# Performance work log

Hardware: AMD Instinct MI355X
Metric: run time of the kernel (lower is better)

Reference implementation:

```python
import jax, jax.numpy as jnp
import numpy as np

N = 50000      # nodes
E = 800000     # directed edges (before self loops)
IN = 128       # in_channels
H = 4          # heads
C = 64         # hidden_channels per head
G = 64         # graphs in batch
SLOPE = 0.2    # PyG GATConv default negative_slope


def setup_inputs() -> dict:
    key = jax.random.key(0)
    ks = jax.random.split(key, 16)
    x = jax.random.normal(ks[0], (N, IN), jnp.float32)
    edge_index = jax.random.randint(ks[1], (2, E), 0, N, dtype=jnp.int32)
    batch = jnp.sort(jax.random.randint(ks[2], (N,), 0, G, dtype=jnp.int32))
    s_in = 1.0 / np.sqrt(IN)
    s_hid = 1.0 / np.sqrt(H * C)
    return {
        "x": x,
        "edge_index": edge_index,
        "batch": batch,
        # layer 1: GATConv(IN -> C, heads=H, concat)
        "W1": jax.random.normal(ks[3], (IN, H * C), jnp.float32) * s_in,
        "a_src1": jax.random.normal(ks[4], (H, C), jnp.float32) * s_hid,
        "a_dst1": jax.random.normal(ks[5], (H, C), jnp.float32) * s_hid,
        "b1": jnp.zeros((H * C,), jnp.float32),
        # layer 2: GATConv(H*C -> C, heads=H, concat)
        "W2": jax.random.normal(ks[6], (H * C, H * C), jnp.float32) * s_hid,
        "a_src2": jax.random.normal(ks[7], (H, C), jnp.float32) * s_hid,
        "a_dst2": jax.random.normal(ks[8], (H, C), jnp.float32) * s_hid,
        "b2": jnp.zeros((H * C,), jnp.float32),
        # classifier head
        "W_lin": jax.random.normal(ks[9], (H * C, 2), jnp.float32) * s_hid,
        "b_lin": jnp.zeros((2,), jnp.float32),
    }


def _gat_conv(x, src, dst, W, a_src, a_dst, b):
    """PyG-style GATConv (concat heads, self-loops already in src/dst)."""
    n = x.shape[0]
    h = (x @ W).reshape(n, H, C)                       # [n, H, C]
    alpha_s = jnp.einsum('nhc,hc->nh', h, a_src)       # [n, H]
    alpha_d = jnp.einsum('nhc,hc->nh', h, a_dst)
    e = alpha_s[src] + alpha_d[dst]                    # [Etot, H]
    e = jnp.where(e > 0, e, SLOPE * e)                 # LeakyReLU
    # segment softmax over edges incoming to each destination node
    e_max = jax.lax.stop_gradient(jax.ops.segment_max(e, dst, num_segments=n))
    ex = jnp.exp(e - e_max[dst])
    denom = jax.ops.segment_sum(ex, dst, num_segments=n)
    alpha = ex / denom[dst]                            # [Etot, H]
    msg = alpha[:, :, None] * h[src]                   # [Etot, H, C]
    out = jax.ops.segment_sum(msg, dst, num_segments=n)
    return out.reshape(n, H * C) + b


def reference(x, edge_index, batch, W1, a_src1, a_dst1, b1,
              W2, a_src2, a_dst2, b2, W_lin, b_lin):
    n = x.shape[0]
    # add self loops (PyG GATConv default add_self_loops=True)
    loop = jnp.arange(n, dtype=edge_index.dtype)
    src = jnp.concatenate([edge_index[0], loop])
    dst = jnp.concatenate([edge_index[1], loop])

    h = _gat_conv(x, src, dst, W1, a_src1, a_dst1, b1)
    h = jax.nn.elu(h)                                  # dropout inactive (eval)
    h = _gat_conv(h, src, dst, W2, a_src2, a_dst2, b2)
    h = jax.nn.elu(h)

    # global mean pool over node-to-graph assignment
    sums = jax.ops.segment_sum(h, batch, num_segments=G)
    cnt = jax.ops.segment_sum(jnp.ones((n,), h.dtype), batch, num_segments=G)
    pooled = sums / jnp.maximum(cnt, 1.0)[:, None]     # [G, H*C]

    return pooled @ W_lin + b_lin                      # [G, 2] logits
```

## Files before the change

kernel.cpp:

```cpp
#include <hip/hip_runtime.h>
#include <hip/hip_bf16.h>
#include <math.h>

#define NN 50000
#define EE 800000
#define IN_CH 128
#define HH 4
#define CC 64
#define GG 64
#define HC 256
#define SLOPE 0.2f

#define NBUK 98
#define BDST 512
#define CAPB 10240
#define CAPD 64

typedef short bf16x8 __attribute__((ext_vector_type(8)));
typedef float f32x4  __attribute__((ext_vector_type(4)));
typedef float f32x2  __attribute__((ext_vector_type(2)));

__device__ inline ushort f2bf(float f) {
    union { __hip_bfloat16 h; ushort u; } c;
    c.h = __float2bfloat16(f);
    return c.u;
}
__device__ inline float bfu(ushort u) {
    union { uint u; float f; } c; c.u = ((uint)u) << 16; return c.f;
}
__device__ inline uchar f2e4m3(float v) {
    return (uchar)(__builtin_amdgcn_cvt_pk_fp8_f32(v, v, 0, false) & 0xff);
}
__device__ inline void pkfma(f32x2& a, f32x2 b, f32x2 c) {
    asm("v_pk_fma_f32 %0, %1, %2, %0" : "+v"(a) : "v"(b), "v"(c));
}


__global__ void init_kernel(int* __restrict__ bcnt,
                            float* __restrict__ pool, float* __restrict__ pcnt) {
    int i = blockIdx.x * blockDim.x + threadIdx.x;
    if (i < NBUK) bcnt[i] = 0;
    if (i < GG * HC) pool[i] = 0.f;
    if (i < GG) pcnt[i] = 0.f;
}


__global__ __launch_bounds__(256) void partition_kernel(const int* __restrict__ ei,
                                                        int* __restrict__ bcnt,
                                                        int2* __restrict__ part,
                                                        int total) {
    __shared__ int hist[NBUK];
    __shared__ int base[NBUK];
    int t = threadIdx.x;
    int c0 = blockIdx.x * 2048;
    for (int b = t; b < NBUK; b += 256) hist[b] = 0;
    __syncthreads();
    int s[8], d[8], rk[8], bk[8];
    #pragma unroll
    for (int k = 0; k < 8; ++k) {
        int i = c0 + k * 256 + t;
        rk[k] = -1;
        if (i < total) {
            if (i < EE) { s[k] = ei[i]; d[k] = ei[EE + i]; }
            else        { s[k] = d[k] = i - EE; }
            bk[k] = d[k] >> 9;
            rk[k] = atomicAdd(&hist[bk[k]], 1);
        }
    }
    __syncthreads();
    for (int b = t; b < NBUK; b += 256) {
        int h = hist[b];
        base[b] = h ? atomicAdd(&bcnt[b], h) : 0;
    }
    __syncthreads();
    #pragma unroll
    for (int k = 0; k < 8; ++k) {
        if (rk[k] >= 0) {
            int pos = base[bk[k]] + rk[k];
            if (pos < CAPB)
                part[(size_t)bk[k] * CAPB + pos] = make_int2(s[k], d[k]);
        }
    }
}


__global__ __launch_bounds__(1024) void bucket_csr_kernel(const int* __restrict__ bcnt,
                                                          const int2* __restrict__ part,
                                                          ushort* __restrict__ csrb,
                                                          int* __restrict__ cnt_out, int n) {
    __shared__ int cnt[BDST];
    int b = blockIdx.x, t = threadIdx.x;
    int d0 = b << 9;
    for (int i = t; i < BDST; i += 1024) cnt[i] = 0;
    __syncthreads();
    int m = min(bcnt[b], CAPB);
    const int2* pp = part + (size_t)b * CAPB;
    for (int i = t; i < m; i += 1024) {
        int2 e = pp[i];
        int ld = e.y - d0;
        int r = atomicAdd(&cnt[ld], 1);
        if (r < CAPD)
            csrb[((size_t)(d0 + ld) << 6) + r] = (ushort)e.x;
    }
    __syncthreads();
    for (int i = t; i < BDST; i += 1024) {
        int dd = d0 + i;
        if (dd < n) cnt_out[dd] = min(cnt[i], CAPD);
    }
}


__global__ __launch_bounds__(256) void convert_w_kernel(const float* __restrict__ B,
                                                        ushort* __restrict__ Bt, int K) {
    __shared__ float tile[32][33];
    int kt = blockIdx.x;
    int n0 = blockIdx.y * 32;
    int tx = threadIdx.x & 31, ty = threadIdx.x >> 5;
    #pragma unroll
    for (int r = ty; r < 32; r += 8)
        tile[r][tx] = B[(size_t)(kt * 32 + r) * 256 + n0 + tx];
    __syncthreads();
    #pragma unroll
    for (int r = ty; r < 32; r += 8)
        Bt[((size_t)kt * 256 + n0 + r) * 32 + tx] = f2bf(tile[tx][r]);
}


template <int K, bool A_BF16>
__global__ __launch_bounds__(256) void mfma_gemm_fused(const void* __restrict__ Ap,
                                                       const ushort* __restrict__ Bt,
                                                       uchar* __restrict__ H8,
                                                       float* __restrict__ as_,
                                                       float* __restrict__ ad_,
                                                       const float* __restrict__ a_src,
                                                       const float* __restrict__ a_dst,
                                                       int M) {
    __shared__ __align__(16) ushort As[64 * 32];
    __shared__ __align__(16) ushort Bs[256 * 32];
    int tid = threadIdx.x;
    int wave = tid >> 6, lane = tid & 63;
    int bm = blockIdx.x * 64;

    f32x4 acc[4][4] = {{}};

    for (int k0 = 0; k0 < K; k0 += 32) {
        {
            int row = tid >> 2, sl = tid & 3;
            int gr = bm + row;
            uint4 q = {0u, 0u, 0u, 0u};
            if (gr < M) {
                if constexpr (A_BF16) {
                    q = *reinterpret_cast<const uint4*>((const ushort*)Ap + (size_t)gr * K + k0 + sl * 8);
                } else {
                    const float* ap = (const float*)Ap + (size_t)gr * K + k0 + sl * 8;
                    float4 f0 = *reinterpret_cast<const float4*>(ap);
                    float4 f1 = *reinterpret_cast<const float4*>(ap + 4);
                    q.x = (uint)f2bf(f0.x) | ((uint)f2bf(f0.y) << 16);
                    q.y = (uint)f2bf(f0.z) | ((uint)f2bf(f0.w) << 16);
                    q.z = (uint)f2bf(f1.x) | ((uint)f2bf(f1.y) << 16);
                    q.w = (uint)f2bf(f1.z) | ((uint)f2bf(f1.w) << 16);
                }
            }
            int ssl = sl ^ ((row >> 1) & 3);
            *reinterpret_cast<uint4*>(&As[row * 32 + ssl * 8]) = q;
        }
        {
            const ushort* bt = Bt + (size_t)(k0 >> 5) * (256 * 32);
            #pragma unroll
            for (int cI = 0; cI < 4; ++cI) {
                int idx = cI * 256 + tid;
                uint4 v = *reinterpret_cast<const uint4*>(bt + idx * 8);
                int n = idx >> 2, sl = idx & 3;
                int ssl = sl ^ ((n >> 1) & 3);
                *reinterpret_cast<uint4*>(&Bs[n * 32 + ssl * 8]) = v;
            }
        }
        __syncthreads();

        int r16 = lane & 15, kg = lane >> 4;
        bf16x8 af[4], bfr[4];
        #pragma unroll
        for (int mi = 0; mi < 4; ++mi) {
            int row = mi * 16 + r16;
            int ssl = kg ^ ((row >> 1) & 3);
            af[mi] = *reinterpret_cast<const bf16x8*>(&As[row * 32 + ssl * 8]);
        }
        #pragma unroll
        for (int ni = 0; ni < 4; ++ni) {
            int n = wave * 64 + ni * 16 + r16;
            int ssl = kg ^ ((n >> 1) & 3);
            bfr[ni] = *reinterpret_cast<const bf16x8*>(&Bs[n * 32 + ssl * 8]);
        }
        #pragma unroll
        for (int mi = 0; mi < 4; ++mi)
            #pragma unroll
            for (int ni = 0; ni < 4; ++ni)
                acc[mi][ni] = __builtin_amdgcn_mfma_f32_16x16x32_bf16(af[mi], bfr[ni], acc[mi][ni], 0, 0, 0);
        __syncthreads();
    }

    int r16 = lane & 15, rg = lane >> 4;
    float asv[4], adv[4];
    #pragma unroll
    for (int ni = 0; ni < 4; ++ni) {
        asv[ni] = a_src[wave * 64 + ni * 16 + r16];
        adv[ni] = a_dst[wave * 64 + ni * 16 + r16];
    }
    #pragma unroll
    for (int mi = 0; mi < 4; ++mi) {
        #pragma unroll
        for (int r = 0; r < 4; ++r) {
            int row = bm + mi * 16 + rg * 4 + r;
            float ps = 0.f, pd = 0.f;
            if (row < M) {
                #pragma unroll
                for (int ni = 0; ni < 4; ++ni) {
                    float v = acc[mi][ni][r];
                    H8[(size_t)row * HC + wave * 64 + ni * 16 + r16] = f2e4m3(v);
                    ps += v * asv[ni];
                    pd += v * adv[ni];
                }
            }
            #pragma unroll
            for (int o = 1; o < 16; o <<= 1) {
                ps += __shfl_xor(ps, o, 64);
                pd += __shfl_xor(pd, o, 64);
            }
            if (row < M && r16 == 0) {
                as_[row * HH + wave] = ps;
                ad_[row * HH + wave] = pd;
            }
        }
    }
}


template <bool OUT_BF16>
__global__ __launch_bounds__(256) void aggregate14_kernel(const uchar* __restrict__ h8,
                                                          const float* __restrict__ as_,
                                                          const float* __restrict__ ad_,
                                                          const int* __restrict__ cnt,
                                                          const ushort* __restrict__ csrb,
                                                          const float* __restrict__ bias,
                                                          void* __restrict__ outp, int n) {
    int w = threadIdx.x >> 6, lane = threadIdx.x & 63;
    int dst = blockIdx.x * 4 + w;
    if (dst >= n) return;
    int es = lane >> 2, hh = lane & 3;
    int ep = lane >> 5, cl = lane & 31;
    int hsel = cl >> 3;

    __shared__ int2 s_pk[4][64][4];

    int deg = cnt[dst];
    int degp = (deg + 7) & ~7;
    const ushort* srcs = csrb + ((size_t)dst << 6);
    float ad = ad_[dst * HH + hh];

    f32x2 accp[4] = {};
    const char* hb = (const char*)h8 + cl * 8;

    int ntile = (degp + 15) >> 4;

    {
        float ew[4]; int sw[4];
        float lm = -INFINITY;
        #pragma unroll
        for (int t = 0; t < 4; ++t) {
            int j = t * 16 + es;
            float e = -INFINITY; int s = 0;
            if (t < ntile && j < deg) {
                s = (int)srcs[j];
                float tv = as_[s * HH + hh] + ad;
                e = fmaxf(tv, tv * SLOPE);
            }
            ew[t] = e; sw[t] = s;
            lm = fmaxf(lm, e);
        }
        #pragma unroll
        for (int o = 4; o < 64; o <<= 1) lm = fmaxf(lm, __shfl_xor(lm, o, 64));
        float den = 0.f;
        #pragma unroll
        for (int t = 0; t < 4; ++t) {
            float wgt = __expf(ew[t] - lm);
            ew[t] = wgt; den += wgt;
        }
        #pragma unroll
        for (int o = 4; o < 64; o <<= 1) den += __shfl_xor(den, o, 64);
        float invden = 1.f / den;
        #pragma unroll
        for (int t = 0; t < 4; ++t) {
            int j = t * 16 + es;
            if (t < ntile && j < degp) {
                s_pk[w][j][hh] = make_int2(__float_as_int(ew[t] * invden), sw[t] << 8);
            }
        }
    }

#define LOADPK(off_, vv, al)                                             \
    {                                                                    \
        int2 pk_ = s_pk[w][jj + (off_) + ep][hsel];                      \
        al = __int_as_float(pk_.x);                                      \
        vv = *reinterpret_cast<const uint2*>(hb + pk_.y);                \
    }

#define DECODE_PK(vv, al)                                                \
    {                                                                    \
        f32x2 ap_; ap_[0] = al; ap_[1] = al;                             \
        f32x2 f_;                                                        \
        f_ = __builtin_amdgcn_cvt_pk_f32_fp8((int)(vv).x, false);        \
        pkfma(accp[0], f_, ap_);                                         \
        f_ = __builtin_amdgcn_cvt_pk_f32_fp8((int)(vv).x, true);         \
        pkfma(accp[1], f_, ap_);                                         \
        f_ = __builtin_amdgcn_cvt_pk_f32_fp8((int)(vv).y, false);        \
        pkfma(accp[2], f_, ap_);                                         \
        f_ = __builtin_amdgcn_cvt_pk_f32_fp8((int)(vv).y, true);         \
        pkfma(accp[3], f_, ap_);                                         \
    }

    for (int jj = 0; jj < degp; jj += 8) {
        uint2 v0, v1, v2, v3;
        float a0, a1, a2, a3;
        LOADPK(0, v0, a0)
        LOADPK(2, v1, a1)
        LOADPK(4, v2, a2)
        LOADPK(6, v3, a3)
        DECODE_PK(v0, a0)
        DECODE_PK(v1, a1)
        DECODE_PK(v2, a2)
        DECODE_PK(v3, a3)
    }
#undef LOADPK
#undef DECODE_PK

    float lo[4] = {accp[0][0], accp[0][1], accp[1][0], accp[1][1]};
    float hi[4] = {accp[2][0], accp[2][1], accp[3][0], accp[3][1]};
    float fin[4];
    #pragma unroll
    for (int k = 0; k < 4; ++k) {
        float send = ep ? lo[k] : hi[k];
        float recv = __shfl_xor(send, 32, 64);
        fin[k] = (ep ? hi[k] : lo[k]) + recv;
    }

    int ch = cl * 8 + ep * 4;
    const float4 b4 = *reinterpret_cast<const float4*>(bias + ch);
    float r0 = fin[0] + b4.x, r1 = fin[1] + b4.y, r2 = fin[2] + b4.z, r3 = fin[3] + b4.w;
    r0 = r0 > 0.f ? r0 : __expf(r0) - 1.f;
    r1 = r1 > 0.f ? r1 : __expf(r1) - 1.f;
    r2 = r2 > 0.f ? r2 : __expf(r2) - 1.f;
    r3 = r3 > 0.f ? r3 : __expf(r3) - 1.f;
    if constexpr (OUT_BF16) {
        uint2 q;
        q.x = (uint)f2bf(r0) | ((uint)f2bf(r1) << 16);
        q.y = (uint)f2bf(r2) | ((uint)f2bf(r3) << 16);
        *reinterpret_cast<uint2*>((ushort*)outp + (size_t)dst * HC + ch) = q;
    } else {
        *reinterpret_cast<float4*>((float*)outp + (size_t)dst * HC + ch) =
            make_float4(r0, r1, r2, r3);
    }
}


__global__ __launch_bounds__(256) void pool_kernel(const ushort* __restrict__ o,
                                                   const int* __restrict__ batch,
                                                   float* __restrict__ pool,
                                                   float* __restrict__ pcnt, int n) {
    int t = threadIdx.x;
    int start = blockIdx.x * 64;
    if (start >= n) return;
    int endn = min(start + 64, n);
    int g = batch[start];
    float acc = 0.f;
    int cnt = 0;
    for (int node = start; node < endn; ++node) {
        int gb = batch[node];
        if (gb != g) {
            atomicAdd(&pool[g * HC + t], acc);
            if (t == 0) atomicAdd(&pcnt[g], (float)cnt);
            acc = 0.f; cnt = 0; g = gb;
        }
        acc += bfu(o[(size_t)node * HC + t]);
        cnt++;
    }
    atomicAdd(&pool[g * HC + t], acc);
    if (t == 0) atomicAdd(&pcnt[g], (float)cnt);
}

__global__ __launch_bounds__(256) void head_kernel(const float* __restrict__ pool,
                                                   const float* __restrict__ pcnt,
                                                   const float* __restrict__ Wl,
                                                   const float* __restrict__ bl,
                                                   float* __restrict__ out) {
    int g = blockIdx.x;
    int t = threadIdx.x;
    float inv = 1.f / fmaxf(pcnt[g], 1.f);
    float p = pool[g * HC + t] * inv;
    float v0 = p * Wl[t * 2 + 0];
    float v1 = p * Wl[t * 2 + 1];
    #pragma unroll
    for (int o = 32; o > 0; o >>= 1) {
        v0 += __shfl_down(v0, o, 64);
        v1 += __shfl_down(v1, o, 64);
    }
    __shared__ float s0[4], s1[4];
    int wid = t >> 6, lane = t & 63;
    if (lane == 0) { s0[wid] = v0; s1[wid] = v1; }
    __syncthreads();
    if (t == 0) {
        out[g * 2 + 0] = s0[0] + s0[1] + s0[2] + s0[3] + bl[0];
        out[g * 2 + 1] = s1[0] + s1[1] + s1[2] + s1[3] + bl[1];
    }
}


extern "C" void kernel_launch(void* const* d_in, const int* in_sizes, int n_in,
                              void* d_out, int out_size, void* d_ws, size_t ws_size,
                              hipStream_t stream) {
    const float* x    = (const float*)d_in[0];
    const int*   ei   = (const int*)d_in[1];
    const int*   batch= (const int*)d_in[2];
    const float* W1   = (const float*)d_in[3];
    const float* as1  = (const float*)d_in[4];
    const float* ad1  = (const float*)d_in[5];
    const float* b1   = (const float*)d_in[6];
    const float* W2   = (const float*)d_in[7];
    const float* as2  = (const float*)d_in[8];
    const float* ad2  = (const float*)d_in[9];
    const float* b2   = (const float*)d_in[10];
    const float* Wl   = (const float*)d_in[11];
    const float* bl   = (const float*)d_in[12];
    float* out = (float*)d_out;

    char* ws = (char*)d_ws;
    size_t off_b = 0;
    auto alloc = [&](size_t bytes) -> void* {
        void* p = ws + off_b;
        off_b = (off_b + bytes + 255) & ~(size_t)255;
        return p;
    };
    uchar*  h8   = (uchar*)alloc((size_t)NN * HC);
    ushort* o1   = (ushort*)alloc((size_t)NN * HC * 2);
    ushort* o2   = (ushort*)alloc((size_t)NN * HC * 2);
    float*  as_  = (float*)alloc((size_t)NN * HH * 4);
    float*  ad_  = (float*)alloc((size_t)NN * HH * 4);
    int*    bcnt = (int*)alloc((size_t)NBUK * 4);
    int2*   part = (int2*)alloc((size_t)NBUK * CAPB * 8);
    ushort* csrb = (ushort*)alloc((size_t)NN * CAPD * 2);
    int*    cnt  = (int*)alloc((size_t)NN * 4);
    float*  pool = (float*)alloc((size_t)GG * HC * 4);
    float*  pcnt = (float*)alloc((size_t)GG * 4);
    ushort* Bt1  = (ushort*)alloc((size_t)HC * IN_CH * 2);
    ushort* Bt2  = (ushort*)alloc((size_t)HC * HC * 2);
    if (off_b > ws_size) return;

    const int TOTAL = EE + NN;

    init_kernel<<<(GG * HC + 255) / 256, 256, 0, stream>>>(bcnt, pool, pcnt);
    partition_kernel<<<(TOTAL + 2047) / 2048, 256, 0, stream>>>(ei, bcnt, part, TOTAL);
    bucket_csr_kernel<<<NBUK, 1024, 0, stream>>>(bcnt, part, csrb, cnt, NN);

    convert_w_kernel<<<dim3(IN_CH / 32, 8), 256, 0, stream>>>(W1, Bt1, IN_CH);
    convert_w_kernel<<<dim3(HC / 32, 8), 256, 0, stream>>>(W2, Bt2, HC);

    int gblocks = (NN + 63) / 64;
    int ablocks = (NN + 3) / 4;
    mfma_gemm_fused<IN_CH, false><<<gblocks, 256, 0, stream>>>(x, Bt1, h8, as_, ad_, as1, ad1, NN);
    aggregate14_kernel<true><<<ablocks, 256, 0, stream>>>(h8, as_, ad_, cnt, csrb, b1, o1, NN);
    mfma_gemm_fused<HC, true><<<gblocks, 256, 0, stream>>>(o1, Bt2, h8, as_, ad_, as2, ad2, NN);
    aggregate14_kernel<true><<<ablocks, 256, 0, stream>>>(h8, as_, ad_, cnt, csrb, b2, o2, NN);
    pool_kernel<<<(NN + 63) / 64, 256, 0, stream>>>(o2, batch, pool, pcnt, NN);
    head_kernel<<<GG, 256, 0, stream>>>(pool, pcnt, Wl, bl, out);
}
```

Measured before the change: 192.4 us.

## Merge prep kernels, stage CSR rows in LDS, fuse pooling with head

Combines bucket-counter init and both weight transposes into one prep kernel. Builds per-bucket CSR rows in shared memory and writes them out with coalesced 16-byte stores. Replaces the atomic pool kernel and the head kernel with a single per-graph kernel that binary-searches the sorted batch array and sums its node range. This reduces launches and scattered writes, but pooling now runs on only 64 blocks with a serial loop per graph, and bucket_csr uses 64KB of LDS.

```diff
diff --git a/kernel.cpp b/kernel.cpp
--- a/kernel.cpp
+++ b/kernel.cpp
@@ -36,12 +36,34 @@
 }
 
 
-__global__ void init_kernel(int* __restrict__ bcnt,
-                            float* __restrict__ pool, float* __restrict__ pcnt) {
-    int i = blockIdx.x * blockDim.x + threadIdx.x;
-    if (i < NBUK) bcnt[i] = 0;
-    if (i < GG * HC) pool[i] = 0.f;
-    if (i < GG) pcnt[i] = 0.f;
+__device__ void conv_body(const float* __restrict__ B, ushort* __restrict__ Bt,
+                          int kt, int n0, float (*tile)[33]) {
+    int tx = threadIdx.x & 31, ty = threadIdx.x >> 5;
+    #pragma unroll
+    for (int r = ty; r < 32; r += 8)
+        tile[r][tx] = B[(size_t)(kt * 32 + r) * 256 + n0 + tx];
+    __syncthreads();
+    #pragma unroll
+    for (int r = ty; r < 32; r += 8)
+        Bt[((size_t)kt * 256 + n0 + r) * 32 + tx] = f2bf(tile[tx][r]);
+}
+
+__global__ __launch_bounds__(256) void prep_kernel(const float* __restrict__ W1,
+                                                   ushort* __restrict__ Bt1,
+                                                   const float* __restrict__ W2,
+                                                   ushort* __restrict__ Bt2,
+                                                   int* __restrict__ bcnt) {
+    __shared__ float tile[32][33];
+    int b = blockIdx.x;
+    if (b < 32) {
+        conv_body(W1, Bt1, b >> 3, (b & 7) * 32, tile);
+    } else if (b < 96) {
+        int bb = b - 32;
+        conv_body(W2, Bt2, bb >> 3, (bb & 7) * 32, tile);
+    } else {
+        int i = threadIdx.x;
+        if (i < NBUK) bcnt[i] = 0;
+    }
 }
 
 
@@ -89,6 +111,7 @@
                                                           ushort* __restrict__ csrb,
                                                           int* __restrict__ cnt_out, int n) {
     __shared__ int cnt[BDST];
+    __shared__ ushort rows[BDST * CAPD];
     int b = blockIdx.x, t = threadIdx.x;
     int d0 = b << 9;
     for (int i = t; i < BDST; i += 1024) cnt[i] = 0;
@@ -99,30 +122,17 @@
         int2 e = pp[i];
         int ld = e.y - d0;
         int r = atomicAdd(&cnt[ld], 1);
-        if (r < CAPD)
-            csrb[((size_t)(d0 + ld) << 6) + r] = (ushort)e.x;
-    }
-    __syncthreads();
+        if (r < CAPD) rows[(ld << 6) + r] = (ushort)e.x;
+    }
+    __syncthreads();
+    const uint4* src4 = reinterpret_cast<const uint4*>(rows);
+    uint4* dst4 = reinterpret_cast<uint4*>(csrb + ((size_t)d0 << 6));
+    #pragma unroll
+    for (int i = 0; i < 4; ++i) dst4[i * 1024 + t] = src4[i * 1024 + t];
     for (int i = t; i < BDST; i += 1024) {
         int dd = d0 + i;
         if (dd < n) cnt_out[dd] = min(cnt[i], CAPD);
     }
-}
-
-
-__global__ __launch_bounds__(256) void convert_w_kernel(const float* __restrict__ B,
-                                                        ushort* __restrict__ Bt, int K) {
-    __shared__ float tile[32][33];
-    int kt = blockIdx.x;
-    int n0 = blockIdx.y * 32;
-    int tx = threadIdx.x & 31, ty = threadIdx.x >> 5;
-    #pragma unroll
-    for (int r = ty; r < 32; r += 8)
-        tile[r][tx] = B[(size_t)(kt * 32 + r) * 256 + n0 + tx];
-    __syncthreads();
-    #pragma unroll
-    for (int r = ty; r < 32; r += 8)
-        Bt[((size_t)kt * 256 + n0 + r) * 32 + tx] = f2bf(tile[tx][r]);
 }
 
 
@@ -362,46 +372,32 @@
 }
 
 
-__global__ __launch_bounds__(256) void pool_kernel(const ushort* __restrict__ o,
-                                                   const int* __restrict__ batch,
-                                                   float* __restrict__ pool,
-                                                   float* __restrict__ pcnt, int n) {
-    int t = threadIdx.x;
-    int start = blockIdx.x * 64;
-    if (start >= n) return;
-    int endn = min(start + 64, n);
-    int g = batch[start];
-    float acc = 0.f;
-    int cnt = 0;
-    for (int node = start; node < endn; ++node) {
-        int gb = batch[node];
-        if (gb != g) {
-            atomicAdd(&pool[g * HC + t], acc);
-            if (t == 0) atomicAdd(&pcnt[g], (float)cnt);
-            acc = 0.f; cnt = 0; g = gb;
-        }
-        acc += bfu(o[(size_t)node * HC + t]);
-        cnt++;
-    }
-    atomicAdd(&pool[g * HC + t], acc);
-    if (t == 0) atomicAdd(&pcnt[g], (float)cnt);
-}
-
-__global__ __launch_bounds__(256) void head_kernel(const float* __restrict__ pool,
-                                                   const float* __restrict__ pcnt,
-                                                   const float* __restrict__ Wl,
-                                                   const float* __restrict__ bl,
-                                                   float* __restrict__ out) {
+__global__ __launch_bounds__(256) void pool_head_kernel(const ushort* __restrict__ o,
+                                                        const int* __restrict__ batch,
+                                                        const float* __restrict__ Wl,
+                                                        const float* __restrict__ bl,
+                                                        float* __restrict__ out, int n) {
     int g = blockIdx.x;
     int t = threadIdx.x;
-    float inv = 1.f / fmaxf(pcnt[g], 1.f);
-    float p = pool[g * HC + t] * inv;
+    int lo = 0, hi = n;
+    while (lo < hi) { int mid = (lo + hi) >> 1; if (batch[mid] < g) lo = mid + 1; else hi = mid; }
+    int start = lo;
+    hi = n;
+    while (lo < hi) { int mid = (lo + hi) >> 1; if (batch[mid] < g + 1) lo = mid + 1; else hi = mid; }
+    int end = lo;
+
+    float acc = 0.f;
+    #pragma unroll 4
+    for (int node = start; node < end; ++node)
+        acc += bfu(o[(size_t)node * HC + t]);
+    float inv = 1.f / fmaxf((float)(end - start), 1.f);
+    float p = acc * inv;
     float v0 = p * Wl[t * 2 + 0];
     float v1 = p * Wl[t * 2 + 1];
     #pragma unroll
-    for (int o = 32; o > 0; o >>= 1) {
-        v0 += __shfl_down(v0, o, 64);
-        v1 += __shfl_down(v1, o, 64);
+    for (int off = 32; off > 0; off >>= 1) {
+        v0 += __shfl_down(v0, off, 64);
+        v1 += __shfl_down(v1, off, 64);
     }
     __shared__ float s0[4], s1[4];
     int wid = t >> 6, lane = t & 63;
@@ -446,22 +442,17 @@
     float*  ad_  = (float*)alloc((size_t)NN * HH * 4);
     int*    bcnt = (int*)alloc((size_t)NBUK * 4);
     int2*   part = (int2*)alloc((size_t)NBUK * CAPB * 8);
-    ushort* csrb = (ushort*)alloc((size_t)NN * CAPD * 2);
+    ushort* csrb = (ushort*)alloc((size_t)NBUK * BDST * CAPD * 2);
     int*    cnt  = (int*)alloc((size_t)NN * 4);
-    float*  pool = (float*)alloc((size_t)GG * HC * 4);
-    float*  pcnt = (float*)alloc((size_t)GG * 4);
     ushort* Bt1  = (ushort*)alloc((size_t)HC * IN_CH * 2);
     ushort* Bt2  = (ushort*)alloc((size_t)HC * HC * 2);
     if (off_b > ws_size) return;
 
     const int TOTAL = EE + NN;
 
-    init_kernel<<<(GG * HC + 255) / 256, 256, 0, stream>>>(bcnt, pool, pcnt);
+    prep_kernel<<<97, 256, 0, stream>>>(W1, Bt1, W2, Bt2, bcnt);
     partition_kernel<<<(TOTAL + 2047) / 2048, 256, 0, stream>>>(ei, bcnt, part, TOTAL);
     bucket_csr_kernel<<<NBUK, 1024, 0, stream>>>(bcnt, part, csrb, cnt, NN);
-
-    convert_w_kernel<<<dim3(IN_CH / 32, 8), 256, 0, stream>>>(W1, Bt1, IN_CH);
-    convert_w_kernel<<<dim3(HC / 32, 8), 256, 0, stream>>>(W2, Bt2, HC);
 
     int gblocks = (NN + 63) / 64;
     int ablocks = (NN + 3) / 4;
@@ -469,6 +460,5 @@
     aggregate14_kernel<true><<<ablocks, 256, 0, stream>>>(h8, as_, ad_, cnt, csrb, b1, o1, NN);
     mfma_gemm_fused<HC, true><<<gblocks, 256, 0, stream>>>(o1, Bt2, h8, as_, ad_, as2, ad2, NN);
     aggregate14_kernel<true><<<ablocks, 256, 0, stream>>>(h8, as_, ad_, cnt, csrb, b2, o2, NN);
-    pool_kernel<<<(NN + 63) / 64, 256, 0, stream>>>(o2, batch, pool, pcnt, NN);
-    head_kernel<<<GG, 256, 0, stream>>>(pool, pcnt, Wl, bl, out);
-}
+    pool_head_kernel<<<GG, 256, 0, stream>>>(o2, batch, Wl, bl, out, NN);
+}
```

New measurement: 220.2 us. 1.14x slower.
